# Performance work log

Measured on AMD Instinct MI355X. Metric: run time of the kernel, lower is better.

## Reference

```python
import jax, jax.numpy as jnp
import numpy as np

B, T, D_IN, D_LAT, N_UNITS = 2048, 200, 64, 64, 100


def setup_inputs() -> dict:
    key = jax.random.key(0)
    ks = jax.random.split(key, 20)
    s = 0.05
    inp = {
        "data": jax.random.normal(ks[0], (B, T, D_IN), dtype=jnp.float32),
        "time_steps": jnp.arange(T, dtype=jnp.float32),
        # ODE func: 2-layer MLP latent -> n_units -> latent (tanh hidden)
        "Wf1": jax.random.normal(ks[1], (D_LAT, N_UNITS), jnp.float32) * s,
        "bf1": jnp.zeros((N_UNITS,), jnp.float32),
        "Wf2": jax.random.normal(ks[2], (N_UNITS, D_LAT), jnp.float32) * s,
        "bf2": jnp.zeros((D_LAT,), jnp.float32),
        # GRU update gate net: [latent+input] -> n_units -> latent
        "Wz1": jax.random.normal(ks[3], (D_LAT + D_IN, N_UNITS), jnp.float32) * s,
        "bz1": jnp.zeros((N_UNITS,), jnp.float32),
        "Wz2": jax.random.normal(ks[4], (N_UNITS, D_LAT), jnp.float32) * s,
        "bz2": jnp.zeros((D_LAT,), jnp.float32),
        # GRU reset gate net
        "Wr1": jax.random.normal(ks[5], (D_LAT + D_IN, N_UNITS), jnp.float32) * s,
        "br1": jnp.zeros((N_UNITS,), jnp.float32),
        "Wr2": jax.random.normal(ks[6], (N_UNITS, D_LAT), jnp.float32) * s,
        "br2": jnp.zeros((D_LAT,), jnp.float32),
        # GRU candidate-state net
        "Wh1": jax.random.normal(ks[7], (D_LAT + D_IN, N_UNITS), jnp.float32) * s,
        "bh1": jnp.zeros((N_UNITS,), jnp.float32),
        "Wh2": jax.random.normal(ks[8], (N_UNITS, D_LAT), jnp.float32) * s,
        "bh2": jnp.zeros((D_LAT,), jnp.float32),
    }
    return inp


def _mlp(x, W1, b1, W2, b2):
    return jnp.tanh(x @ W1 + b1) @ W2 + b2


def reference(data, time_steps, Wf1, bf1, Wf2, bf2,
              Wz1, bz1, Wz2, bz2, Wr1, br1, Wr2, br2,
              Wh1, bh1, Wh2, bh2):
    n_traj = data.shape[0]
    latent_dim = Wf1.shape[0]
    prev_y0 = jnp.zeros((n_traj, latent_dim), dtype=data.dtype)

    # Faithful to original control flow: with uniform arange time steps,
    # |prev_t - t_i| < minimum_step always holds -> single explicit Euler step.
    # Original code swaps (prev_t, t_i) at the end of each iteration, so the
    # effective dt at iteration i is: i==1 -> ts[1]-ts[0]; i>=2 -> ts[i-2]-ts[i-1].
    dts = jnp.concatenate([time_steps[1:2] - time_steps[0:1],
                           time_steps[:-2] - time_steps[1:-1]])  # [T-1]

    xs_data = jnp.moveaxis(data[:, 1:, :], 0, 1)  # [T-1, B, D_in]

    def step(prev_y, inp):
        x, dt = inp
        # Euler step of the neural ODE
        yi_ode = prev_y + _mlp(prev_y, Wf1, bf1, Wf2, bf2) * dt
        # GRU update (GRUUnitOriginal): gates from concat(y_ode, x)
        c = jnp.concatenate([yi_ode, x], axis=-1)
        z = jax.nn.sigmoid(_mlp(c, Wz1, bz1, Wz2, bz2))
        r = jax.nn.sigmoid(_mlp(c, Wr1, br1, Wr2, br2))
        ch = jnp.concatenate([yi_ode * r, x], axis=-1)
        h = jnp.tanh(_mlp(ch, Wh1, bh1, Wh2, bh2))
        y = (1.0 - z) * h + z * yi_ode
        return y, y

    yi, ys = jax.lax.scan(step, prev_y0, (xs_data, dts))
    latent_ys = jnp.moveaxis(ys, 0, 1)  # [B, T-1, latent]
    return yi, latent_ys
```

## Files before the change

kernel.cpp:

```cpp
#include <hip/hip_runtime.h>


#define NBT   2048
#define TSTEP 200
#define NT    8

typedef short s8v __attribute__((ext_vector_type(8)));
typedef float f4v __attribute__((ext_vector_type(4)));

#define RB_Y 144
#define RB_C 272
#define OFF_Y  0
#define OFF_C  2304
#define OFF_HF 6656
#define OFF_HZ 11008
#define OFF_HR 15360
#define OFF_HH 19712
#define SMEM_TOT 24064

__device__ __forceinline__ unsigned cvtpk(float lo, float hi) {
    unsigned r;
    asm("v_cvt_pk_bf16_f32 %0, %1, %2" : "=v"(r) : "v"(lo), "v"(hi));
    return r;
}
__device__ __forceinline__ unsigned short f2bf(float f) {
    unsigned int b = __float_as_uint(f);
    return (unsigned short)((b + 0x7fffu + ((b >> 16) & 1u)) >> 16);
}
__device__ __forceinline__ float bf2f(unsigned short u) {
    return __uint_as_float(((unsigned)u) << 16);
}
__device__ __forceinline__ float tanh_f(float x) {
    float e = __expf(2.0f * x);
    return fmaf(-2.0f, __builtin_amdgcn_rcpf(e + 1.0f), 1.0f);
}
__device__ __forceinline__ float sigm_f(float x) {
    return __builtin_amdgcn_rcpf(1.0f + __expf(-x));
}
__device__ __forceinline__ f4v mfma16(s8v a, s8v b, f4v c) {
    return __builtin_amdgcn_mfma_f32_16x16x32_bf16(a, b, c, 0, 0, 0);
}
__device__ __forceinline__ f4v splat(float b) { f4v v = {b, b, b, b}; return v; }

__device__ __forceinline__ s8v load_bfrag(const float* __restrict__ W,
                                          int Ncols, int Krows, int k0, int n) {
    s8v r;
#pragma unroll
    for (int j = 0; j < 8; ++j) {
        const int k = k0 + j;
        const float v = (k < Krows && n < Ncols) ? W[k * Ncols + n] : 0.0f;
        r[j] = (short)f2bf(v);
    }
    return r;
}

template <int RB>
__device__ __forceinline__ s8v load_af(const char* base, int lane, int kt) {
    return *(const s8v*)(base + (lane & 15) * RB + ((lane >> 4) * 16) + kt * 64);
}

__device__ __forceinline__ void store4(char* base, int col2, int rb, int pitch,
                                       float v0, float v1, float v2, float v3) {
    const unsigned u01 = cvtpk(v0, v1), u23 = cvtpk(v2, v3);
    *(short*)(base + (rb + 0) * pitch + col2) = (short)(u01 & 0xffffu);
    *(short*)(base + (rb + 1) * pitch + col2) = (short)(u01 >> 16);
    *(short*)(base + (rb + 2) * pitch + col2) = (short)(u23 & 0xffffu);
    *(short*)(base + (rb + 3) * pitch + col2) = (short)(u23 >> 16);
}
__device__ __forceinline__ void store_tanh(char* base, int n0, int lane, f4v a) {
    store4(base, (n0 + (lane & 15)) * 2, (lane >> 4) * 4, RB_C,
           tanh_f(a[0]), tanh_f(a[1]), tanh_f(a[2]), tanh_f(a[3]));
}

__global__ __launch_bounds__(512, 2) void ode_rnn_mfma8(
    const float* __restrict__ data, const float* __restrict__ tsv,
    const float* __restrict__ Wf1, const float* __restrict__ bf1,
    const float* __restrict__ Wf2, const float* __restrict__ bf2,
    const float* __restrict__ Wz1, const float* __restrict__ bz1,
    const float* __restrict__ Wz2, const float* __restrict__ bz2,
    const float* __restrict__ Wr1, const float* __restrict__ br1,
    const float* __restrict__ Wr2, const float* __restrict__ br2,
    const float* __restrict__ Wh1, const float* __restrict__ bh1,
    const float* __restrict__ Wh2, const float* __restrict__ bh2,
    float* __restrict__ out_yi, float* __restrict__ out_ys)
{
    __shared__ __align__(16) char smem[SMEM_TOT];

    const int tid  = threadIdx.x;
    const int lane = tid & 63;
    const int wv   = tid >> 6;
    const bool isA = (wv < 4);
    const int b0   = blockIdx.x * NT;

    for (int i = tid; i < SMEM_TOT / 4; i += 512) ((unsigned*)smem)[i] = 0u;

    const int kb = (lane >> 4) * 8;
    const int n1 = wv * 16 + (lane & 15);
    const int n2 = (wv & 3) * 16 + (lane & 15);

    s8v Bf1[2], Bz1[4], Br1[4], Bh1[4];
    s8v Bf2[4], Bz2[4], Bh2[4], Br2[4];
#pragma unroll
    for (int kt = 0; kt < 2; ++kt)
        Bf1[kt] = load_bfrag(Wf1, 100, 64, kt * 32 + kb, n1);
#pragma unroll
    for (int kt = 0; kt < 4; ++kt) {
        Bz1[kt] = load_bfrag(Wz1, 100, 128, kt * 32 + kb, n1);
        Br1[kt] = load_bfrag(Wr1, 100, 128, kt * 32 + kb, n1);
        Bh1[kt] = load_bfrag(Wh1, 100, 128, kt * 32 + kb, n1);
    }
    if (isA) {
#pragma unroll
        for (int kt = 0; kt < 4; ++kt) {
            Bf2[kt] = load_bfrag(Wf2, 64, 100, kt * 32 + kb, n2);
            Bz2[kt] = load_bfrag(Wz2, 64, 100, kt * 32 + kb, n2);
            Bh2[kt] = load_bfrag(Wh2, 64, 100, kt * 32 + kb, n2);
        }
    } else {
#pragma unroll
        for (int kt = 0; kt < 4; ++kt)
            Br2[kt] = load_bfrag(Wr2, 64, 100, kt * 32 + kb, n2);
    }

    const float b1f = (n1 < 100) ? bf1[n1] : 0.0f;
    const float b1z = (n1 < 100) ? bz1[n1] : 0.0f;
    const float b1r = (n1 < 100) ? br1[n1] : 0.0f;
    const float b1h = (n1 < 100) ? bh1[n1] : 0.0f;
    const float bF2 = isA ? bf2[n2] : 0.0f;
    const float bZ2 = isA ? bz2[n2] : 0.0f;
    const float bH2 = isA ? bh2[n2] : 0.0f;
    const float bR2 = isA ? 0.0f : br2[n2];

    const int t2  = tid & 255;
    const int xtr = t2 >> 5;
    const int xd  = (t2 & 31) * 2;

    const int col2 = n2 * 2;
    const int rb   = (lane >> 4) * 4;

    f4v y_reg = splat(0.0f), yode = splat(0.0f), zf = splat(0.0f);
    __syncthreads();

    for (int s = 0; s < TSTEP - 1; ++s) {
        float2 xv;
        if (!isA)
            xv = *(const float2*)&data[((size_t)(b0 + xtr) * TSTEP + (s + 1)) * 64 + xd];
        const float dt = (s == 0) ? (tsv[1] - tsv[0]) : (tsv[s - 1] - tsv[s]);

        {
            const s8v ya0 = load_af<RB_Y>(smem + OFF_Y, lane, 0);
            const s8v ya1 = load_af<RB_Y>(smem + OFF_Y, lane, 1);
            f4v a = splat(b1f);
            a = mfma16(ya0, Bf1[0], a);
            a = mfma16(ya1, Bf1[1], a);
            store_tanh(smem + OFF_HF, wv * 16, lane, a);
        }
        __syncthreads();

        if (isA) {
            f4v ac = splat(bF2);
#pragma unroll
            for (int kt = 0; kt < 4; ++kt)
                ac = mfma16(load_af<RB_C>(smem + OFF_HF, lane, kt), Bf2[kt], ac);
#pragma unroll
            for (int r = 0; r < 4; ++r) yode[r] = fmaf(dt, ac[r], y_reg[r]);
            store4(smem + OFF_C, col2, rb, RB_C, yode[0], yode[1], yode[2], yode[3]);
        } else {
            *(unsigned*)(smem + OFF_C + xtr * RB_C + 128 + (t2 & 31) * 4) =
                cvtpk(xv.x, xv.y);
        }
        __syncthreads();

        {
            const s8v c0 = load_af<RB_C>(smem + OFF_C, lane, 0);
            const s8v c1 = load_af<RB_C>(smem + OFF_C, lane, 1);
            const s8v c2 = load_af<RB_C>(smem + OFF_C, lane, 2);
            const s8v c3 = load_af<RB_C>(smem + OFF_C, lane, 3);
            f4v az = splat(b1z), ar = splat(b1r);
            az = mfma16(c0, Bz1[0], az); az = mfma16(c1, Bz1[1], az);
            az = mfma16(c2, Bz1[2], az); az = mfma16(c3, Bz1[3], az);
            ar = mfma16(c0, Br1[0], ar); ar = mfma16(c1, Br1[1], ar);
            ar = mfma16(c2, Br1[2], ar); ar = mfma16(c3, Br1[3], ar);
            store_tanh(smem + OFF_HZ, wv * 16, lane, az);
            store_tanh(smem + OFF_HR, wv * 16, lane, ar);
        }
        __syncthreads();

        if (isA) {
            f4v az = splat(bZ2);
#pragma unroll
            for (int kt = 0; kt < 4; ++kt)
                az = mfma16(load_af<RB_C>(smem + OFF_HZ, lane, kt), Bz2[kt], az);
#pragma unroll
            for (int r = 0; r < 4; ++r) zf[r] = sigm_f(az[r]);
        } else {
            f4v ar = splat(bR2);
#pragma unroll
            for (int kt = 0; kt < 4; ++kt)
                ar = mfma16(load_af<RB_C>(smem + OFF_HR, lane, kt), Br2[kt], ar);
            float ch[4];
#pragma unroll
            for (int r = 0; r < 4; ++r) {
                const unsigned short yv =
                    *(const unsigned short*)(smem + OFF_C + (rb + r) * RB_C + col2);
                ch[r] = bf2f(yv) * sigm_f(ar[r]);
            }
            store4(smem + OFF_C, col2, rb, RB_C, ch[0], ch[1], ch[2], ch[3]);
        }
        __syncthreads();

        {
            const s8v d0 = load_af<RB_C>(smem + OFF_C, lane, 0);
            const s8v d1 = load_af<RB_C>(smem + OFF_C, lane, 1);
            const s8v d2 = load_af<RB_C>(smem + OFF_C, lane, 2);
            const s8v d3 = load_af<RB_C>(smem + OFF_C, lane, 3);
            f4v ah = splat(b1h);
            ah = mfma16(d0, Bh1[0], ah); ah = mfma16(d1, Bh1[1], ah);
            ah = mfma16(d2, Bh1[2], ah); ah = mfma16(d3, Bh1[3], ah);
            store_tanh(smem + OFF_HH, wv * 16, lane, ah);
        }
        __syncthreads();

        if (isA) {
            f4v ah = splat(bH2);
#pragma unroll
            for (int kt = 0; kt < 4; ++kt)
                ah = mfma16(load_af<RB_C>(smem + OFF_HH, lane, kt), Bh2[kt], ah);
#pragma unroll
            for (int r = 0; r < 4; ++r) {
                const float h = tanh_f(ah[r]);
                y_reg[r] = (1.0f - zf[r]) * h + zf[r] * yode[r];
            }
            store4(smem + OFF_Y, col2, rb, RB_Y, y_reg[0], y_reg[1], y_reg[2], y_reg[3]);
            if (lane < 32) {
#pragma unroll
                for (int r = 0; r < 4; ++r) {
                    const int row = rb + r;
                    out_ys[((size_t)(b0 + row) * (TSTEP - 1) + s) * 64 + n2] = y_reg[r];
                }
                if (s == TSTEP - 2) {
#pragma unroll
                    for (int r = 0; r < 4; ++r)
                        out_yi[(size_t)(b0 + rb + r) * 64 + n2] = y_reg[r];
                }
            }
        }
        __syncthreads();
    }
}

extern "C" void kernel_launch(void* const* d_in, const int* in_sizes, int n_in,
                              void* d_out, int out_size, void* d_ws, size_t ws_size,
                              hipStream_t stream) {
    const float* data = (const float*)d_in[0];
    const float* tsv  = (const float*)d_in[1];
    const float* Wf1 = (const float*)d_in[2];  const float* bf1 = (const float*)d_in[3];
    const float* Wf2 = (const float*)d_in[4];  const float* bf2 = (const float*)d_in[5];
    const float* Wz1 = (const float*)d_in[6];  const float* bz1 = (const float*)d_in[7];
    const float* Wz2 = (const float*)d_in[8];  const float* bz2 = (const float*)d_in[9];
    const float* Wr1 = (const float*)d_in[10]; const float* br1 = (const float*)d_in[11];
    const float* Wr2 = (const float*)d_in[12]; const float* br2 = (const float*)d_in[13];
    const float* Wh1 = (const float*)d_in[14]; const float* bh1 = (const float*)d_in[15];
    const float* Wh2 = (const float*)d_in[16]; const float* bh2 = (const float*)d_in[17];

    float* out_yi = (float*)d_out;
    float* out_ys = out_yi + (size_t)NBT * 64;

    ode_rnn_mfma8<<<NBT / NT, 512, 0, stream>>>(
        data, tsv, Wf1, bf1, Wf2, bf2, Wz1, bz1, Wz2, bz2,
        Wr1, br1, Wr2, br2, Wh1, bh1, Wh2, bh2, out_yi, out_ys);
}
```

Before: 355.5 us.

## Stage second-layer weights in LDS to cut registers and raise occupancy

Moves the four second-layer weight matrices out of per-thread registers into transposed bf16 copies in dynamic shared memory, read per MFMA. Launch bounds go from 2 to 4 blocks per CU. The 8-row batch now maps only to rows 0-7 of each MFMA tile, so only half-wave stores are kept, and hidden buffers for f and h share one region. The output store is deferred by one step to overlap with compute, and dt is carried forward. This trades extra LDS reads and a much larger LDS footprint (~79KB, which may itself cap occupancy) for lower register pressure.

```diff
diff --git a/kernel.cpp b/kernel.cpp
--- a/kernel.cpp
+++ b/kernel.cpp
@@ -8,15 +8,19 @@
 typedef short s8v __attribute__((ext_vector_type(8)));
 typedef float f4v __attribute__((ext_vector_type(4)));
 
+#define RB_W 272
 #define RB_Y 144
 #define RB_C 272
-#define OFF_Y  0
-#define OFF_C  2304
-#define OFF_HF 6656
-#define OFF_HZ 11008
-#define OFF_HR 15360
-#define OFF_HH 19712
-#define SMEM_TOT 24064
+#define OFF_WF2 0
+#define OFF_WZ2 17408
+#define OFF_WR2 34816
+#define OFF_WH2 52224
+#define OFF_Y   69632
+#define OFF_C   70784
+#define OFF_HFH 72960
+#define OFF_HZ  75136
+#define OFF_HR  77312
+#define SMEM_TOT 79488
 
 __device__ __forceinline__ unsigned cvtpk(float lo, float hi) {
     unsigned r;
@@ -56,7 +60,11 @@
 
 template <int RB>
 __device__ __forceinline__ s8v load_af(const char* base, int lane, int kt) {
-    return *(const s8v*)(base + (lane & 15) * RB + ((lane >> 4) * 16) + kt * 64);
+    return *(const s8v*)(base + (lane & 7) * RB + ((lane >> 4) * 16) + kt * 64);
+}
+__device__ __forceinline__ s8v load_bf(const char* base, int tile, int lane, int kt) {
+    return *(const s8v*)(base + (tile * 16 + (lane & 15)) * RB_W +
+                         ((lane >> 4) * 16) + kt * 64);
 }
 
 __device__ __forceinline__ void store4(char* base, int col2, int rb, int pitch,
@@ -68,11 +76,20 @@
     *(short*)(base + (rb + 3) * pitch + col2) = (short)(u23 >> 16);
 }
 __device__ __forceinline__ void store_tanh(char* base, int n0, int lane, f4v a) {
-    store4(base, (n0 + (lane & 15)) * 2, (lane >> 4) * 4, RB_C,
-           tanh_f(a[0]), tanh_f(a[1]), tanh_f(a[2]), tanh_f(a[3]));
-}
-
-__global__ __launch_bounds__(512, 2) void ode_rnn_mfma8(
+    if (lane < 32)
+        store4(base, (n0 + (lane & 15)) * 2, (lane >> 4) * 4, RB_C,
+               tanh_f(a[0]), tanh_f(a[1]), tanh_f(a[2]), tanh_f(a[3]));
+}
+
+__device__ void stage_w2t(const float* __restrict__ W, char* __restrict__ dst,
+                          int tid) {
+    for (int idx = tid; idx < 6400; idx += 512) {
+        const int k = idx >> 6, n = idx & 63;
+        *(unsigned short*)(dst + n * RB_W + k * 2) = f2bf(W[idx]);
+    }
+}
+
+__global__ __launch_bounds__(512, 4) void ode_rnn_2b(
     const float* __restrict__ data, const float* __restrict__ tsv,
     const float* __restrict__ Wf1, const float* __restrict__ bf1,
     const float* __restrict__ Wf2, const float* __restrict__ bf2,
@@ -84,7 +101,7 @@
     const float* __restrict__ Wh2, const float* __restrict__ bh2,
     float* __restrict__ out_yi, float* __restrict__ out_ys)
 {
-    __shared__ __align__(16) char smem[SMEM_TOT];
+    extern __shared__ __align__(16) char smem[];
 
     const int tid  = threadIdx.x;
     const int lane = tid & 63;
@@ -93,13 +110,18 @@
     const int b0   = blockIdx.x * NT;
 
     for (int i = tid; i < SMEM_TOT / 4; i += 512) ((unsigned*)smem)[i] = 0u;
+    __syncthreads();
+    stage_w2t(Wf2, smem + OFF_WF2, tid);
+    stage_w2t(Wz2, smem + OFF_WZ2, tid);
+    stage_w2t(Wr2, smem + OFF_WR2, tid);
+    stage_w2t(Wh2, smem + OFF_WH2, tid);
 
     const int kb = (lane >> 4) * 8;
     const int n1 = wv * 16 + (lane & 15);
-    const int n2 = (wv & 3) * 16 + (lane & 15);
+    const int tw2 = wv & 3;
+    const int n2  = tw2 * 16 + (lane & 15);
 
     s8v Bf1[2], Bz1[4], Br1[4], Bh1[4];
-    s8v Bf2[4], Bz2[4], Bh2[4], Br2[4];
 #pragma unroll
     for (int kt = 0; kt < 2; ++kt)
         Bf1[kt] = load_bfrag(Wf1, 100, 64, kt * 32 + kb, n1);
@@ -108,18 +130,6 @@
         Bz1[kt] = load_bfrag(Wz1, 100, 128, kt * 32 + kb, n1);
         Br1[kt] = load_bfrag(Wr1, 100, 128, kt * 32 + kb, n1);
         Bh1[kt] = load_bfrag(Wh1, 100, 128, kt * 32 + kb, n1);
-    }
-    if (isA) {
-#pragma unroll
-        for (int kt = 0; kt < 4; ++kt) {
-            Bf2[kt] = load_bfrag(Wf2, 64, 100, kt * 32 + kb, n2);
-            Bz2[kt] = load_bfrag(Wz2, 64, 100, kt * 32 + kb, n2);
-            Bh2[kt] = load_bfrag(Wh2, 64, 100, kt * 32 + kb, n2);
-        }
-    } else {
-#pragma unroll
-        for (int kt = 0; kt < 4; ++kt)
-            Br2[kt] = load_bfrag(Wr2, 64, 100, kt * 32 + kb, n2);
     }
 
     const float b1f = (n1 < 100) ? bf1[n1] : 0.0f;
@@ -137,15 +147,22 @@
 
     const int col2 = n2 * 2;
     const int rb   = (lane >> 4) * 4;
+    const int rbm  = rb & 7;
 
     f4v y_reg = splat(0.0f), yode = splat(0.0f), zf = splat(0.0f);
+    float dt = tsv[1] - tsv[0];
     __syncthreads();
 
     for (int s = 0; s < TSTEP - 1; ++s) {
+        if (isA && s > 0 && lane < 32) {
+#pragma unroll
+            for (int r = 0; r < 4; ++r)
+                out_ys[((size_t)(b0 + rb + r) * (TSTEP - 1) + (s - 1)) * 64 + n2] =
+                    y_reg[r];
+        }
         float2 xv;
         if (!isA)
             xv = *(const float2*)&data[((size_t)(b0 + xtr) * TSTEP + (s + 1)) * 64 + xd];
-        const float dt = (s == 0) ? (tsv[1] - tsv[0]) : (tsv[s - 1] - tsv[s]);
 
         {
             const s8v ya0 = load_af<RB_Y>(smem + OFF_Y, lane, 0);
@@ -153,7 +170,7 @@
             f4v a = splat(b1f);
             a = mfma16(ya0, Bf1[0], a);
             a = mfma16(ya1, Bf1[1], a);
-            store_tanh(smem + OFF_HF, wv * 16, lane, a);
+            store_tanh(smem + OFF_HFH, wv * 16, lane, a);
         }
         __syncthreads();
 
@@ -161,10 +178,13 @@
             f4v ac = splat(bF2);
 #pragma unroll
             for (int kt = 0; kt < 4; ++kt)
-                ac = mfma16(load_af<RB_C>(smem + OFF_HF, lane, kt), Bf2[kt], ac);
+                ac = mfma16(load_af<RB_C>(smem + OFF_HFH, lane, kt),
+                            load_bf(smem + OFF_WF2, tw2, lane, kt), ac);
 #pragma unroll
             for (int r = 0; r < 4; ++r) yode[r] = fmaf(dt, ac[r], y_reg[r]);
-            store4(smem + OFF_C, col2, rb, RB_C, yode[0], yode[1], yode[2], yode[3]);
+            if (lane < 32)
+                store4(smem + OFF_C, col2, rb, RB_C,
+                       yode[0], yode[1], yode[2], yode[3]);
         } else {
             *(unsigned*)(smem + OFF_C + xtr * RB_C + 128 + (t2 & 31) * 4) =
                 cvtpk(xv.x, xv.y);
@@ -190,22 +210,27 @@
             f4v az = splat(bZ2);
 #pragma unroll
             for (int kt = 0; kt < 4; ++kt)
-                az = mfma16(load_af<RB_C>(smem + OFF_HZ, lane, kt), Bz2[kt], az);
+                az = mfma16(load_af<RB_C>(smem + OFF_HZ, lane, kt),
+                            load_bf(smem + OFF_WZ2, tw2, lane, kt), az);
 #pragma unroll
             for (int r = 0; r < 4; ++r) zf[r] = sigm_f(az[r]);
         } else {
+            unsigned short yv[4];
+#pragma unroll
+            for (int r = 0; r < 4; ++r)
+                yv[r] = *(const unsigned short*)
+                    (smem + OFF_C + (rbm + r) * RB_C + col2);
             f4v ar = splat(bR2);
 #pragma unroll
             for (int kt = 0; kt < 4; ++kt)
-                ar = mfma16(load_af<RB_C>(smem + OFF_HR, lane, kt), Br2[kt], ar);
+                ar = mfma16(load_af<RB_C>(smem + OFF_HR, lane, kt),
+                            load_bf(smem + OFF_WR2, tw2, lane, kt), ar);
             float ch[4];
 #pragma unroll
-            for (int r = 0; r < 4; ++r) {
-                const unsigned short yv =
-                    *(const unsigned short*)(smem + OFF_C + (rb + r) * RB_C + col2);
-                ch[r] = bf2f(yv) * sigm_f(ar[r]);
-            }
-            store4(smem + OFF_C, col2, rb, RB_C, ch[0], ch[1], ch[2], ch[3]);
+            for (int r = 0; r < 4; ++r)
+                ch[r] = bf2f(yv[r]) * sigm_f(ar[r]);
+            if (lane < 32)
+                store4(smem + OFF_C, col2, rb, RB_C, ch[0], ch[1], ch[2], ch[3]);
         }
         __syncthreads();
 
@@ -217,7 +242,7 @@
             f4v ah = splat(b1h);
             ah = mfma16(d0, Bh1[0], ah); ah = mfma16(d1, Bh1[1], ah);
             ah = mfma16(d2, Bh1[2], ah); ah = mfma16(d3, Bh1[3], ah);
-            store_tanh(smem + OFF_HH, wv * 16, lane, ah);
+            store_tanh(smem + OFF_HFH, wv * 16, lane, ah);
         }
         __syncthreads();
 
@@ -225,27 +250,28 @@
             f4v ah = splat(bH2);
 #pragma unroll
             for (int kt = 0; kt < 4; ++kt)
-                ah = mfma16(load_af<RB_C>(smem + OFF_HH, lane, kt), Bh2[kt], ah);
+                ah = mfma16(load_af<RB_C>(smem + OFF_HFH, lane, kt),
+                            load_bf(smem + OFF_WH2, tw2, lane, kt), ah);
 #pragma unroll
             for (int r = 0; r < 4; ++r) {
                 const float h = tanh_f(ah[r]);
                 y_reg[r] = (1.0f - zf[r]) * h + zf[r] * yode[r];
             }
-            store4(smem + OFF_Y, col2, rb, RB_Y, y_reg[0], y_reg[1], y_reg[2], y_reg[3]);
-            if (lane < 32) {
-#pragma unroll
-                for (int r = 0; r < 4; ++r) {
-                    const int row = rb + r;
-                    out_ys[((size_t)(b0 + row) * (TSTEP - 1) + s) * 64 + n2] = y_reg[r];
-                }
-                if (s == TSTEP - 2) {
-#pragma unroll
-                    for (int r = 0; r < 4; ++r)
-                        out_yi[(size_t)(b0 + rb + r) * 64 + n2] = y_reg[r];
-                }
-            }
-        }
-        __syncthreads();
+            if (lane < 32)
+                store4(smem + OFF_Y, col2, rb, RB_Y,
+                       y_reg[0], y_reg[1], y_reg[2], y_reg[3]);
+        }
+        dt = tsv[s] - tsv[s + 1];
+        __syncthreads();
+    }
+
+    if (isA && lane < 32) {
+#pragma unroll
+        for (int r = 0; r < 4; ++r) {
+            out_ys[((size_t)(b0 + rb + r) * (TSTEP - 1) + (TSTEP - 2)) * 64 + n2] =
+                y_reg[r];
+            out_yi[(size_t)(b0 + rb + r) * 64 + n2] = y_reg[r];
+        }
     }
 }
 
@@ -266,7 +292,10 @@
     float* out_yi = (float*)d_out;
     float* out_ys = out_yi + (size_t)NBT * 64;
 
-    ode_rnn_mfma8<<<NBT / NT, 512, 0, stream>>>(
+    (void)hipFuncSetAttribute((const void*)ode_rnn_2b,
+                              hipFuncAttributeMaxDynamicSharedMemorySize, SMEM_TOT);
+
+    ode_rnn_2b<<<NBT / NT, 512, SMEM_TOT, stream>>>(
         data, tsv, Wf1, bf1, Wf2, bf2, Wz1, bz1, Wz2, bz2,
         Wr1, br1, Wr2, br2, Wh1, bh1, Wh2, bh2, out_yi, out_ys);
 }
```

Result: slower. 563.1 us (+58.4%).
